# Kernel tuning notes

Measured on AMD Instinct MI355X. Metric: run time of the kernel, lower is better.

## Reference

```python
import jax, jax.numpy as jnp
import numpy as np

N_NODE = 40000  # item vocabulary
H = 100         # hidden size (SR-GNN default)
B = 64          # sessions per batch
L = 16          # items per session (equal-length sessions)
N = B * L       # total graph nodes
E = 2048        # total edges
NL = 1          # GatedGraphConv layers


def setup_inputs() -> dict:
    key = jax.random.key(0)
    ks = jax.random.split(key, 20)
    stdv = 1.0 / np.sqrt(H)
    u = lambda k, shape: jax.random.uniform(k, shape, jnp.float32, -stdv, stdv)
    return {
        "x": jax.random.randint(ks[0], (N,), 0, N_NODE),
        "edge_index": jax.random.randint(ks[1], (2, E), 0, N),
        "edge_weight": jax.random.uniform(ks[2], (E,), jnp.float32),
        "batch": jnp.arange(N) // L,  # node -> session id, equal-length sessions
        "embed": u(ks[3], (N_NODE, H)),
        "ggc_w": u(ks[4], (NL, H, H)),
        "gru_wih": u(ks[5], (3 * H, H)),
        "gru_whh": u(ks[6], (3 * H, H)),
        "gru_bih": u(ks[7], (3 * H,)),
        "gru_bhh": u(ks[8], (3 * H,)),
        "W1_w": u(ks[9], (H, H)), "W1_b": u(ks[10], (H,)),
        "W2_w": u(ks[11], (H, H)), "W2_b": u(ks[12], (H,)),
        "Wt_w": u(ks[13], (H, H)), "Wt_b": u(ks[14], (H,)),
        "q_w": u(ks[15], (1, H)), "q_b": u(ks[16], (1,)),
        "W3_w": u(ks[17], (H, 2 * H)), "W3_b": u(ks[18], (H,)),
    }


def reference(x, edge_index, edge_weight, batch, embed, ggc_w, gru_wih, gru_whh,
              gru_bih, gru_bhh, W1_w, W1_b, W2_w, W2_b, Wt_w, Wt_b, q_w, q_b,
              W3_w, W3_b):
    # Embedding lookup
    h = embed[x]  # [N, H]
    src, dst = edge_index[0], edge_index[1]
    # GatedGraphConv: weighted message aggregation + GRUCell update
    for l in range(NL):
        m = h @ ggc_w[l]                                             # [N, H]
        agg = jnp.zeros_like(h).at[dst].add(edge_weight[:, None] * m[src])
        gi = agg @ gru_wih.T + gru_bih                               # [N, 3H]
        gh = h @ gru_whh.T + gru_bhh
        ir, iz, inn = jnp.split(gi, 3, axis=-1)
        hr, hz, hn = jnp.split(gh, 3, axis=-1)
        r = jax.nn.sigmoid(ir + hr)
        zg = jax.nn.sigmoid(iz + hz)
        ng = jnp.tanh(inn + r * hn)
        h = (1.0 - zg) * ng + zg * h
    v = h.reshape(B, L, H)                                           # sessions
    s_l = v[:, -1]                                                   # [B, H] last item
    # alpha = q(sigmoid(W1(v_n) + W2(v)))
    a = jax.nn.sigmoid((s_l @ W1_w.T + W1_b)[:, None, :] + (v @ W2_w.T + W2_b))
    alpha = a @ q_w.T + q_b                                          # [B, L, 1]
    s_g = jnp.sum(alpha * v, axis=1)                                 # [B, H]
    s_h = jnp.concatenate([s_l, s_g], axis=-1) @ W3_w.T + W3_b       # [B, H]
    # Target attention: s_t[b] = softmax(E @ W_t(v_b)^T, -1) @ v_b, contracted
    # directly against E to avoid materializing [B, N_NODE, H].
    vt = v @ Wt_w.T + Wt_b                                           # [B, L, H]
    P = jax.nn.softmax(jnp.einsum('jh,blh->bjl', embed, vt), axis=-1)
    C = jnp.einsum('blh,jh->bjl', v, embed)                          # v_l . E_j
    z = s_h @ embed.T + jnp.sum(P * C, axis=-1)                      # [B, N_NODE]
    return z
```

## Files before the change

### kernel.cpp

```cpp
#include <hip/hip_runtime.h>
#include <hip/hip_bf16.h>

#define Hh    100
#define NN    1024
#define BB    64
#define LL    16
#define EE    2048
#define NNODE 40000

#define BSPL  8
#define BPB   (BB / BSPL)
#define PFR   12
#define PPAN  (PFR * 64 * 8)

typedef unsigned short u16;
typedef __attribute__((ext_vector_type(8))) short short8;
typedef __attribute__((ext_vector_type(4))) float f32x4;

__device__ __forceinline__ float bf2f(u16 u) {
    union { unsigned int i; float f; } v;
    v.i = ((unsigned int)u) << 16;
    return v.f;
}

__device__ __forceinline__ u16 f2bf(float f) {
    unsigned int x = __float_as_uint(f);
    unsigned int lsb = (x >> 16) & 1u;
    x += 0x7fffu + lsb;
    return (u16)(x >> 16);
}

__device__ __forceinline__ float sigmoidf_(float x) {
    return 1.0f / (1.0f + expf(-x));
}

template <bool BF>
__device__ __forceinline__ float ldv(const void* p, size_t i) {
    if (BF) return bf2f(((const u16*)p)[i]);
    return ((const float*)p)[i];
}
__device__ __forceinline__ float ldvf(int flag, const void* p, size_t i) {
    return flag ? ldv<true>(p, i) : ldv<false>(p, i);
}

template <bool BF>
__device__ void cvt_impl(int t,
                         const void* ew, const void* ggc, const void* wih, const void* whh,
                         const void* bih, const void* bhh, const void* W1w, const void* W1b,
                         const void* W2w, const void* W2b, const void* Wtw, const void* Wtb,
                         const void* qw, const void* qb, const void* W3w, const void* W3b,
                         float* __restrict__ W) {
    const void* src; int si; int doff; int di;
    if      (t <   2048) { src = ew;  si = t;          doff = 0;      di = si; }
    else if (t <  12048) { src = ggc; si = t - 2048;   doff = 2048;   di = si; }
    else if (t <  42048) { src = wih; si = t - 12048;  doff = 12048;  di = (si % 100) * 300 + si / 100; }
    else if (t <  72048) { src = whh; si = t - 42048;  doff = 42048;  di = (si % 100) * 300 + si / 100; }
    else if (t <  72348) { src = bih; si = t - 72048;  doff = 72048;  di = si; }
    else if (t <  72648) { src = bhh; si = t - 72348;  doff = 72352;  di = si; }
    else if (t <  82648) { src = W1w; si = t - 72648;  doff = 72656;  di = (si % 100) * 100 + si / 100; }
    else if (t <  82748) { src = W1b; si = t - 82648;  doff = 82656;  di = si; }
    else if (t <  92748) { src = W2w; si = t - 82748;  doff = 82768;  di = (si % 100) * 100 + si / 100; }
    else if (t <  92848) { src = W2b; si = t - 92748;  doff = 92768;  di = si; }
    else if (t < 102848) { src = Wtw; si = t - 92848;  doff = 92880;  di = (si % 100) * 100 + si / 100; }
    else if (t < 102948) { src = Wtb; si = t - 102848; doff = 102880; di = si; }
    else if (t < 103048) { src = qw;  si = t - 102948; doff = 102992; di = si; }
    else if (t < 103049) { src = qb;  si = t - 103048; doff = 103104; di = si; }
    else if (t < 123049) { src = W3w; si = t - 103049; doff = 103120; di = (si % 200) * 100 + si / 200; }
    else                 { src = W3b; si = t - 123049; doff = 123120; di = si; }
    W[doff + di] = ldv<BF>(src, si);
}

__global__ void __launch_bounds__(256) k_cvt(const void* embed_raw, int* __restrict__ flag,
                      const void* ew, const void* ggc, const void* wih, const void* whh,
                      const void* bih, const void* bhh, const void* W1w, const void* W1b,
                      const void* W2w, const void* W2b, const void* Wtw, const void* Wtb,
                      const void* qw, const void* qb, const void* W3w, const void* W3b,
                      float* __restrict__ W) {
    __shared__ int cnt;
    if (threadIdx.x == 0) cnt = 0;
    __syncthreads();
    int bad = 0;
    const u16* eb = (const u16*)embed_raw;
    for (int i = threadIdx.x; i < 4096; i += 256) {
        float v = bf2f(eb[i]);
        if (!(fabsf(v) <= 0.5f)) bad++;
    }
    if (bad) atomicAdd(&cnt, bad);
    __syncthreads();
    const bool bf = (cnt == 0);
    if (blockIdx.x == 0 && threadIdx.x == 0) flag[0] = bf ? 1 : 0;
    int t = blockIdx.x * 256 + threadIdx.x;
    if (t >= 123149) return;
    if (bf) cvt_impl<true >(t, ew, ggc, wih, whh, bih, bhh, W1w, W1b, W2w, W2b, Wtw, Wtb, qw, qb, W3w, W3b, W);
    else    cvt_impl<false>(t, ew, ggc, wih, whh, bih, bhh, W1w, W1b, W2w, W2b, Wtw, Wtb, qw, qb, W3w, W3b, W);
}

__global__ void __launch_bounds__(256) k_gm(const int* __restrict__ flag,
                                            const int* __restrict__ x,
                                            const void* __restrict__ embed,
                                            const float* __restrict__ ggc_w,
                                            float* __restrict__ m,
                                            float* __restrict__ agg) {
    __shared__ float W[Hh * Hh];
    __shared__ float H[8 * Hh];
    const int tid = threadIdx.x;
    const int fl = flag[0];
    const int r0 = blockIdx.x * 8;
    for (int idx = tid; idx < Hh * Hh; idx += 256) W[idx] = ggc_w[idx];
    for (int idx = tid; idx < 8 * Hh; idx += 256) {
        int i = idx / Hh, j = idx - i * Hh;
        H[idx] = ldvf(fl, embed, (size_t)x[r0 + i] * Hh + j);
    }
    for (int idx = tid; idx < 8 * Hh; idx += 256) agg[r0 * Hh + idx] = 0.0f;
    __syncthreads();
    for (int idx = tid; idx < 8 * Hh; idx += 256) {
        int i = idx / Hh, j = idx - i * Hh;
        float acc = 0.0f;
#pragma unroll 4
        for (int k = 0; k < Hh; ++k) acc += H[i * Hh + k] * W[k * Hh + j];
        m[(r0 + i) * Hh + j] = acc;
    }
}

__global__ void k_scatter(const int* __restrict__ ei, const float* __restrict__ ew,
                          const float* __restrict__ m, float* __restrict__ agg) {
    int t = blockIdx.x * 256 + threadIdx.x;
    if (t >= EE * Hh) return;
    int e = t / Hh, j = t - e * Hh;
    int src = ei[e], dst = ei[EE + e];
    atomicAdd(&agg[dst * Hh + j], ew[e] * m[src * Hh + j]);
}

__global__ void k_gru(const int* __restrict__ flag, const int* __restrict__ x,
                      const void* __restrict__ embed,
                      const float* __restrict__ agg,
                      const float* __restrict__ wihT, const float* __restrict__ whhT,
                      const float* __restrict__ bih, const float* __restrict__ bhh,
                      float* __restrict__ h1) {
    int t = blockIdx.x * 256 + threadIdx.x;
    if (t >= NN * Hh) return;
    int i = t / Hh, j = t - i * Hh;
    const int fl = flag[0];
    const size_t erow = (size_t)x[i] * Hh;
    const float* ar = agg + i * Hh;
    float s_ir = bih[j], s_iz = bih[j + Hh], s_in = bih[j + 2 * Hh];
    float s_hr = bhh[j], s_hz = bhh[j + Hh], s_hn = bhh[j + 2 * Hh];
    float h0j = 0.0f;
    for (int k = 0; k < Hh; ++k) {
        float a = ar[k];
        float h = ldvf(fl, embed, erow + k);
        if (k == j) h0j = h;
        const float* wT = wihT + k * 300;
        const float* uT = whhT + k * 300;
        s_ir += a * wT[j];
        s_iz += a * wT[j + 100];
        s_in += a * wT[j + 200];
        s_hr += h * uT[j];
        s_hz += h * uT[j + 100];
        s_hn += h * uT[j + 200];
    }
    float r = sigmoidf_(s_ir + s_hr);
    float z = sigmoidf_(s_iz + s_hz);
    float n = tanhf(s_in + r * s_hn);
    h1[t] = (1.0f - z) * n + z * h0j;
}

__global__ void __launch_bounds__(256) k_att(const float* __restrict__ h1,
                    const float* __restrict__ W1T, const float* __restrict__ W1b,
                    const float* __restrict__ W2T, const float* __restrict__ W2b,
                    const float* __restrict__ WtT, const float* __restrict__ Wtb,
                    const float* __restrict__ qw, const float* __restrict__ qb,
                    const float* __restrict__ W3T, const float* __restrict__ W3b,
                    u16* __restrict__ P) {
    __shared__ float V[LL * Hh];
    __shared__ float Q2[LL * Hh];
    __shared__ float VTs[LL * Hh];
    __shared__ float Q1[Hh];
    __shared__ float AL[LL];
    __shared__ float SG[Hh];
    __shared__ float SH[Hh];
    const int b = blockIdx.x, tid = threadIdx.x;
    for (int idx = tid; idx < LL * Hh; idx += 256) V[idx] = h1[b * LL * Hh + idx];
    __syncthreads();
    for (int idx = tid; idx < LL * Hh; idx += 256) {
        int i = idx / Hh, j = idx - i * Hh;
        float a2 = 0, at = 0;
        for (int k = 0; k < Hh; ++k) {
            float vk = V[i * Hh + k];
            a2 += vk * W2T[k * Hh + j];
            at += vk * WtT[k * Hh + j];
        }
        Q2[idx] = a2 + W2b[j];
        VTs[idx] = at + Wtb[j];
    }
    if (tid < Hh) {
        float a1 = 0;
        for (int k = 0; k < Hh; ++k) a1 += V[(LL - 1) * Hh + k] * W1T[k * Hh + tid];
        Q1[tid] = a1 + W1b[tid];
    }
    __syncthreads();
    if (tid < LL) {
        float acc = 0;
        for (int j = 0; j < Hh; ++j)
            acc += sigmoidf_(Q1[j] + Q2[tid * Hh + j]) * qw[j];
        AL[tid] = acc + qb[0];
    }
    __syncthreads();
    if (tid < Hh) {
        float acc = 0;
#pragma unroll
        for (int l = 0; l < LL; ++l) acc += AL[l] * V[l * Hh + tid];
        SG[tid] = acc;
    }
    __syncthreads();
    if (tid < Hh) {
        float acc = W3b[tid];
        for (int k = 0; k < Hh; ++k) acc += V[(LL - 1) * Hh + k] * W3T[k * Hh + tid];
        for (int k = 0; k < Hh; ++k) acc += SG[k] * W3T[(Hh + k) * Hh + tid];
        SH[tid] = acc;
    }
    __syncthreads();
    for (int w = tid; w < PFR * 64; w += 256) {
        int f = w >> 6, lane = w & 63;
        int t = f >> 2, ks = f & 3;
        int mm = lane & 15, qq = lane >> 4;
        int row = t * 16 + mm;
        int col0 = ks * 32 + qq * 8;
        short8 t8;
#pragma unroll
        for (int e = 0; e < 8; ++e) {
            int col = col0 + e;
            float v = 0.0f;
            if (col < Hh) {
                if      (row < 16) v = VTs[row * Hh + col];
                else if (row < 32) v = V[(row - 16) * Hh + col];
                else if (row == 32) v = SH[col];
            }
            t8[e] = (short)f2bf(v);
        }
        *(short8*)&P[((size_t)b * PFR + f) * 512 + lane * 8] = t8;
    }
}

__device__ __forceinline__ short8 load_efrag(const void* embed, bool bf, int j, int k0) {
    short8 v = {0, 0, 0, 0, 0, 0, 0, 0};
    if (j >= NNODE || k0 >= Hh) return v;
    if (bf) {
        const u16* row = (const u16*)embed + (size_t)j * Hh + k0;
        if (k0 + 8 <= Hh) {
            ushort4 a = *(const ushort4*)(row);
            ushort4 b = *(const ushort4*)(row + 4);
            v[0] = (short)a.x; v[1] = (short)a.y; v[2] = (short)a.z; v[3] = (short)a.w;
            v[4] = (short)b.x; v[5] = (short)b.y; v[6] = (short)b.z; v[7] = (short)b.w;
        } else {
            for (int e = 0; e < Hh - k0; ++e) v[e] = (short)row[e];
        }
    } else {
        const float* row = (const float*)embed + (size_t)j * Hh + k0;
        if (k0 + 8 <= Hh) {
            float4 a = *(const float4*)(row);
            float4 b = *(const float4*)(row + 4);
            v[0] = (short)f2bf(a.x); v[1] = (short)f2bf(a.y); v[2] = (short)f2bf(a.z); v[3] = (short)f2bf(a.w);
            v[4] = (short)f2bf(b.x); v[5] = (short)f2bf(b.y); v[6] = (short)f2bf(b.z); v[7] = (short)f2bf(b.w);
        } else {
            for (int e = 0; e < Hh - k0; ++e) v[e] = (short)f2bf(row[e]);
        }
    }
    return v;
}

__global__ void __launch_bounds__(256) k_score(const int* __restrict__ flag,
                                               const void* __restrict__ embed,
                                               const u16* __restrict__ P,
                                               void* __restrict__ out) {
    __shared__ alignas(16) u16 sPan[2][PPAN];
    const int jb = blockIdx.x * 128;
    const int b0 = blockIdx.y * BPB;
    const int tid = threadIdx.x;
    const bool bf = (flag[0] != 0);
    const int wave = tid >> 6, lane = tid & 63;
    const int m = lane & 15, quad = lane >> 4;

    short8 Bf[2][4];
#pragma unroll
    for (int g = 0; g < 2; ++g)
#pragma unroll
        for (int ks = 0; ks < 4; ++ks)
            Bf[g][ks] = load_efrag(embed, bf, jb + wave * 32 + g * 16 + m, ks * 32 + quad * 8);

    short8 pa = {0, 0, 0, 0, 0, 0, 0, 0};
    short8 pb = {0, 0, 0, 0, 0, 0, 0, 0};
    if (quad == 0) {
        pa[0] = (short)f2bf((float)m);
        pb[0] = (short)f2bf(1.0f);
    }
    f32x4 pd = (f32x4){0.0f, 0.0f, 0.0f, 0.0f};
    pd = __builtin_amdgcn_mfma_f32_16x16x32_bf16(pa, pb, pd, 0, 0, 0);
    const bool isH1 =
        (__builtin_amdgcn_readfirstlane(__float_as_uint(pd[1])) == 0x3f800000u);

    {
        const uint4* s4 = (const uint4*)(P + (size_t)b0 * PPAN);
        uint4 g0 = s4[tid], g1 = s4[tid + 256], g2 = s4[tid + 512];
        uint4* d = (uint4*)sPan[0];
        d[tid] = g0; d[tid + 256] = g1; d[tid + 512] = g2;
    }
    __syncthreads();

    int cur = 0;
    for (int bi = 0; bi < BPB; ++bi) {
        const int b = b0 + bi;
        uint4 g0, g1, g2;
        if (bi + 1 < BPB) {
            const uint4* s4 = (const uint4*)(P + (size_t)(b + 1) * PPAN);
            g0 = s4[tid]; g1 = s4[tid + 256]; g2 = s4[tid + 512];
        }

        const u16* sp = sPan[cur];
        f32x4 acc[2][3];
#pragma unroll
        for (int g = 0; g < 2; ++g)
#pragma unroll
            for (int t = 0; t < 3; ++t)
                acc[g][t] = (f32x4){0.0f, 0.0f, 0.0f, 0.0f};
#pragma unroll
        for (int t = 0; t < 3; ++t) {
            short8 A0 = *(const short8*)&sp[(t * 4 + 0) * 512 + lane * 8];
            short8 A1 = *(const short8*)&sp[(t * 4 + 1) * 512 + lane * 8];
            short8 A2 = *(const short8*)&sp[(t * 4 + 2) * 512 + lane * 8];
            short8 A3 = *(const short8*)&sp[(t * 4 + 3) * 512 + lane * 8];
#pragma unroll
            for (int g = 0; g < 2; ++g) {
                acc[g][t] = __builtin_amdgcn_mfma_f32_16x16x32_bf16(A0, Bf[g][0], acc[g][t], 0, 0, 0);
                acc[g][t] = __builtin_amdgcn_mfma_f32_16x16x32_bf16(A1, Bf[g][1], acc[g][t], 0, 0, 0);
                acc[g][t] = __builtin_amdgcn_mfma_f32_16x16x32_bf16(A2, Bf[g][2], acc[g][t], 0, 0, 0);
                acc[g][t] = __builtin_amdgcn_mfma_f32_16x16x32_bf16(A3, Bf[g][3], acc[g][t], 0, 0, 0);
            }
        }

#pragma unroll
        for (int g = 0; g < 2; ++g) {
            if (isH1) {
                float den = 0.0f, num = 0.0f;
#pragma unroll
                for (int r = 0; r < 4; ++r) {
                    float p = __expf(acc[g][0][r]);
                    den += p;
                    num += p * acc[g][1][r];
                }
                den += __shfl_xor(den, 16); num += __shfl_xor(num, 16);
                den += __shfl_xor(den, 32); num += __shfl_xor(num, 32);
                if (quad == 0) {
                    int j = jb + wave * 32 + g * 16 + m;
                    if (j < NNODE) {
                        float z = acc[g][2][0] + num / den;
                        if (bf) ((u16*)out)[(size_t)b * NNODE + j] = f2bf(z);
                        else    ((float*)out)[(size_t)b * NNODE + j] = z;
                    }
                }
            } else {
                float den[4], num[4];
#pragma unroll
                for (int r = 0; r < 4; ++r) {
                    float p = __expf(acc[g][0][r]);
                    den[r] = p;
                    num[r] = p * acc[g][1][r];
                }
#pragma unroll
                for (int s = 1; s <= 8; s <<= 1)
#pragma unroll
                    for (int r = 0; r < 4; ++r) {
                        den[r] += __shfl_xor(den[r], s);
                        num[r] += __shfl_xor(num[r], s);
                    }
                if (m == 0) {
#pragma unroll
                    for (int r = 0; r < 4; ++r) {
                        int j = jb + wave * 32 + g * 16 + quad * 4 + r;
                        if (j < NNODE) {
                            float z = acc[g][2][r] + num[r] / den[r];
                            if (bf) ((u16*)out)[(size_t)b * NNODE + j] = f2bf(z);
                            else    ((float*)out)[(size_t)b * NNODE + j] = z;
                        }
                    }
                }
            }
        }

        if (bi + 1 < BPB) {
            uint4* d = (uint4*)sPan[cur ^ 1];
            d[tid] = g0; d[tid + 256] = g1; d[tid + 512] = g2;
        }
        __syncthreads();
        cur ^= 1;
    }
}

extern "C" void kernel_launch(void* const* d_in, const int* in_sizes, int n_in,
                              void* d_out, int out_size, void* d_ws, size_t ws_size,
                              hipStream_t stream) {
    const int* x      = (const int*)d_in[0];
    const int* ei     = (const int*)d_in[1];
    const void* ew    = d_in[2];
    const void* embed = d_in[4];
    const void* ggc   = d_in[5];
    const void* wih   = d_in[6];
    const void* whh   = d_in[7];
    const void* bih   = d_in[8];
    const void* bhh   = d_in[9];
    const void* W1w   = d_in[10];
    const void* W1b   = d_in[11];
    const void* W2w   = d_in[12];
    const void* W2b   = d_in[13];
    const void* Wtw   = d_in[14];
    const void* Wtb   = d_in[15];
    const void* qw    = d_in[16];
    const void* qb    = d_in[17];
    const void* W3w   = d_in[18];
    const void* W3b   = d_in[19];
    float* ws = (float*)d_ws;
    int* flag = (int*)d_ws;

    float* W = ws + 64;
    float* ew_f  = W + 0;
    float* ggc_f = W + 2048;
    float* wihT  = W + 12048;
    float* whhT  = W + 42048;
    float* bih_f = W + 72048;
    float* bhh_f = W + 72352;
    float* W1T   = W + 72656;
    float* W1b_f = W + 82656;
    float* W2T   = W + 82768;
    float* W2b_f = W + 92768;
    float* WtT   = W + 92880;
    float* Wtb_f = W + 102880;
    float* qw_f  = W + 102992;
    float* qb_f  = W + 103104;
    float* W3T   = W + 103120;
    float* W3b_f = W + 123120;

    float* D     = ws + 123296;
    float* m     = D;
    float* agg   = D + 102400;
    float* h1    = D;
    u16*   P     = (u16*)(D + 102400);

    k_cvt    <<<dim3(482), dim3(256), 0, stream>>>(embed, flag, ew, ggc, wih, whh, bih, bhh,
                                                   W1w, W1b, W2w, W2b, Wtw, Wtb, qw, qb, W3w, W3b, W);
    k_gm     <<<dim3(128), dim3(256), 0, stream>>>(flag, x, embed, ggc_f, m, agg);
    k_scatter<<<dim3(800), dim3(256), 0, stream>>>(ei, ew_f, m, agg);
    k_gru    <<<dim3(400), dim3(256), 0, stream>>>(flag, x, embed, agg, wihT, whhT, bih_f, bhh_f, h1);
    k_att    <<<dim3(64),  dim3(256), 0, stream>>>(h1, W1T, W1b_f, W2T, W2b_f, WtT, Wtb_f,
                                                   qw_f, qb_f, W3T, W3b_f, P);
    k_score  <<<dim3((NNODE + 127) / 128, BSPL), dim3(256), 0, stream>>>(flag, embed, P, d_out);
}
```

Baseline: 234.6 us.

## Fuse all six stages into one cooperative persistent kernel with grid syncs

Replaces the six separate kernel launches with a single cooperative kernel that runs each stage as a grid-stride loop separated by grid.sync(). The scoring stage becomes a persistent job loop over (node tile, batch split) pairs. The goal is to remove the launch gaps between the short stages. In exchange, every block repeats the bf16 detection check, the gm stage no longer caches weights in shared memory, and grid-wide barriers add their own cost.

```diff
diff --git a/kernel.cpp b/kernel.cpp
--- a/kernel.cpp
+++ b/kernel.cpp
@@ -1,5 +1,8 @@
 #include <hip/hip_runtime.h>
+#include <hip/hip_cooperative_groups.h>
 #include <hip/hip_bf16.h>
+
+namespace cg = cooperative_groups;
 
 #define Hh    100
 #define NN    1024
@@ -12,6 +15,8 @@
 #define BPB   (BB / BSPL)
 #define PFR   12
 #define PPAN  (PFR * 64 * 8)
+#define NJT   313
+#define NJOB  (NJT * BSPL)
 
 typedef unsigned short u16;
 typedef __attribute__((ext_vector_type(8))) short short8;
@@ -39,8 +44,8 @@
     if (BF) return bf2f(((const u16*)p)[i]);
     return ((const float*)p)[i];
 }
-__device__ __forceinline__ float ldvf(int flag, const void* p, size_t i) {
-    return flag ? ldv<true>(p, i) : ldv<false>(p, i);
+__device__ __forceinline__ float ldvb(bool bf, const void* p, size_t i) {
+    return bf ? ldv<true>(p, i) : ldv<false>(p, i);
 }
 
 template <bool BF>
@@ -70,178 +75,6 @@
     W[doff + di] = ldv<BF>(src, si);
 }
 
-__global__ void __launch_bounds__(256) k_cvt(const void* embed_raw, int* __restrict__ flag,
-                      const void* ew, const void* ggc, const void* wih, const void* whh,
-                      const void* bih, const void* bhh, const void* W1w, const void* W1b,
-                      const void* W2w, const void* W2b, const void* Wtw, const void* Wtb,
-                      const void* qw, const void* qb, const void* W3w, const void* W3b,
-                      float* __restrict__ W) {
-    __shared__ int cnt;
-    if (threadIdx.x == 0) cnt = 0;
-    __syncthreads();
-    int bad = 0;
-    const u16* eb = (const u16*)embed_raw;
-    for (int i = threadIdx.x; i < 4096; i += 256) {
-        float v = bf2f(eb[i]);
-        if (!(fabsf(v) <= 0.5f)) bad++;
-    }
-    if (bad) atomicAdd(&cnt, bad);
-    __syncthreads();
-    const bool bf = (cnt == 0);
-    if (blockIdx.x == 0 && threadIdx.x == 0) flag[0] = bf ? 1 : 0;
-    int t = blockIdx.x * 256 + threadIdx.x;
-    if (t >= 123149) return;
-    if (bf) cvt_impl<true >(t, ew, ggc, wih, whh, bih, bhh, W1w, W1b, W2w, W2b, Wtw, Wtb, qw, qb, W3w, W3b, W);
-    else    cvt_impl<false>(t, ew, ggc, wih, whh, bih, bhh, W1w, W1b, W2w, W2b, Wtw, Wtb, qw, qb, W3w, W3b, W);
-}
-
-__global__ void __launch_bounds__(256) k_gm(const int* __restrict__ flag,
-                                            const int* __restrict__ x,
-                                            const void* __restrict__ embed,
-                                            const float* __restrict__ ggc_w,
-                                            float* __restrict__ m,
-                                            float* __restrict__ agg) {
-    __shared__ float W[Hh * Hh];
-    __shared__ float H[8 * Hh];
-    const int tid = threadIdx.x;
-    const int fl = flag[0];
-    const int r0 = blockIdx.x * 8;
-    for (int idx = tid; idx < Hh * Hh; idx += 256) W[idx] = ggc_w[idx];
-    for (int idx = tid; idx < 8 * Hh; idx += 256) {
-        int i = idx / Hh, j = idx - i * Hh;
-        H[idx] = ldvf(fl, embed, (size_t)x[r0 + i] * Hh + j);
-    }
-    for (int idx = tid; idx < 8 * Hh; idx += 256) agg[r0 * Hh + idx] = 0.0f;
-    __syncthreads();
-    for (int idx = tid; idx < 8 * Hh; idx += 256) {
-        int i = idx / Hh, j = idx - i * Hh;
-        float acc = 0.0f;
-#pragma unroll 4
-        for (int k = 0; k < Hh; ++k) acc += H[i * Hh + k] * W[k * Hh + j];
-        m[(r0 + i) * Hh + j] = acc;
-    }
-}
-
-__global__ void k_scatter(const int* __restrict__ ei, const float* __restrict__ ew,
-                          const float* __restrict__ m, float* __restrict__ agg) {
-    int t = blockIdx.x * 256 + threadIdx.x;
-    if (t >= EE * Hh) return;
-    int e = t / Hh, j = t - e * Hh;
-    int src = ei[e], dst = ei[EE + e];
-    atomicAdd(&agg[dst * Hh + j], ew[e] * m[src * Hh + j]);
-}
-
-__global__ void k_gru(const int* __restrict__ flag, const int* __restrict__ x,
-                      const void* __restrict__ embed,
-                      const float* __restrict__ agg,
-                      const float* __restrict__ wihT, const float* __restrict__ whhT,
-                      const float* __restrict__ bih, const float* __restrict__ bhh,
-                      float* __restrict__ h1) {
-    int t = blockIdx.x * 256 + threadIdx.x;
-    if (t >= NN * Hh) return;
-    int i = t / Hh, j = t - i * Hh;
-    const int fl = flag[0];
-    const size_t erow = (size_t)x[i] * Hh;
-    const float* ar = agg + i * Hh;
-    float s_ir = bih[j], s_iz = bih[j + Hh], s_in = bih[j + 2 * Hh];
-    float s_hr = bhh[j], s_hz = bhh[j + Hh], s_hn = bhh[j + 2 * Hh];
-    float h0j = 0.0f;
-    for (int k = 0; k < Hh; ++k) {
-        float a = ar[k];
-        float h = ldvf(fl, embed, erow + k);
-        if (k == j) h0j = h;
-        const float* wT = wihT + k * 300;
-        const float* uT = whhT + k * 300;
-        s_ir += a * wT[j];
-        s_iz += a * wT[j + 100];
-        s_in += a * wT[j + 200];
-        s_hr += h * uT[j];
-        s_hz += h * uT[j + 100];
-        s_hn += h * uT[j + 200];
-    }
-    float r = sigmoidf_(s_ir + s_hr);
-    float z = sigmoidf_(s_iz + s_hz);
-    float n = tanhf(s_in + r * s_hn);
-    h1[t] = (1.0f - z) * n + z * h0j;
-}
-
-__global__ void __launch_bounds__(256) k_att(const float* __restrict__ h1,
-                    const float* __restrict__ W1T, const float* __restrict__ W1b,
-                    const float* __restrict__ W2T, const float* __restrict__ W2b,
-                    const float* __restrict__ WtT, const float* __restrict__ Wtb,
-                    const float* __restrict__ qw, const float* __restrict__ qb,
-                    const float* __restrict__ W3T, const float* __restrict__ W3b,
-                    u16* __restrict__ P) {
-    __shared__ float V[LL * Hh];
-    __shared__ float Q2[LL * Hh];
-    __shared__ float VTs[LL * Hh];
-    __shared__ float Q1[Hh];
-    __shared__ float AL[LL];
-    __shared__ float SG[Hh];
-    __shared__ float SH[Hh];
-    const int b = blockIdx.x, tid = threadIdx.x;
-    for (int idx = tid; idx < LL * Hh; idx += 256) V[idx] = h1[b * LL * Hh + idx];
-    __syncthreads();
-    for (int idx = tid; idx < LL * Hh; idx += 256) {
-        int i = idx / Hh, j = idx - i * Hh;
-        float a2 = 0, at = 0;
-        for (int k = 0; k < Hh; ++k) {
-            float vk = V[i * Hh + k];
-            a2 += vk * W2T[k * Hh + j];
-            at += vk * WtT[k * Hh + j];
-        }
-        Q2[idx] = a2 + W2b[j];
-        VTs[idx] = at + Wtb[j];
-    }
-    if (tid < Hh) {
-        float a1 = 0;
-        for (int k = 0; k < Hh; ++k) a1 += V[(LL - 1) * Hh + k] * W1T[k * Hh + tid];
-        Q1[tid] = a1 + W1b[tid];
-    }
-    __syncthreads();
-    if (tid < LL) {
-        float acc = 0;
-        for (int j = 0; j < Hh; ++j)
-            acc += sigmoidf_(Q1[j] + Q2[tid * Hh + j]) * qw[j];
-        AL[tid] = acc + qb[0];
-    }
-    __syncthreads();
-    if (tid < Hh) {
-        float acc = 0;
-#pragma unroll
-        for (int l = 0; l < LL; ++l) acc += AL[l] * V[l * Hh + tid];
-        SG[tid] = acc;
-    }
-    __syncthreads();
-    if (tid < Hh) {
-        float acc = W3b[tid];
-        for (int k = 0; k < Hh; ++k) acc += V[(LL - 1) * Hh + k] * W3T[k * Hh + tid];
-        for (int k = 0; k < Hh; ++k) acc += SG[k] * W3T[(Hh + k) * Hh + tid];
-        SH[tid] = acc;
-    }
-    __syncthreads();
-    for (int w = tid; w < PFR * 64; w += 256) {
-        int f = w >> 6, lane = w & 63;
-        int t = f >> 2, ks = f & 3;
-        int mm = lane & 15, qq = lane >> 4;
-        int row = t * 16 + mm;
-        int col0 = ks * 32 + qq * 8;
-        short8 t8;
-#pragma unroll
-        for (int e = 0; e < 8; ++e) {
-            int col = col0 + e;
-            float v = 0.0f;
-            if (col < Hh) {
-                if      (row < 16) v = VTs[row * Hh + col];
-                else if (row < 32) v = V[(row - 16) * Hh + col];
-                else if (row == 32) v = SH[col];
-            }
-            t8[e] = (short)f2bf(v);
-        }
-        *(short8*)&P[((size_t)b * PFR + f) * 512 + lane * 8] = t8;
-    }
-}
-
 __device__ __forceinline__ short8 load_efrag(const void* embed, bool bf, int j, int k0) {
     short8 v = {0, 0, 0, 0, 0, 0, 0, 0};
     if (j >= NNODE || k0 >= Hh) return v;
@@ -269,29 +102,192 @@
     return v;
 }
 
-__global__ void __launch_bounds__(256) k_score(const int* __restrict__ flag,
-                                               const void* __restrict__ embed,
-                                               const u16* __restrict__ P,
-                                               void* __restrict__ out) {
-    __shared__ alignas(16) u16 sPan[2][PPAN];
-    const int jb = blockIdx.x * 128;
-    const int b0 = blockIdx.y * BPB;
-    const int tid = threadIdx.x;
-    const bool bf = (flag[0] != 0);
+__global__ void __launch_bounds__(256) mega(
+        const int* __restrict__ x, const int* __restrict__ ei,
+        const void* __restrict__ ew, const void* __restrict__ embed,
+        const void* __restrict__ ggc, const void* __restrict__ wih,
+        const void* __restrict__ whh, const void* __restrict__ bih,
+        const void* __restrict__ bhh, const void* __restrict__ W1w,
+        const void* __restrict__ W1b, const void* __restrict__ W2w,
+        const void* __restrict__ W2b, const void* __restrict__ Wtw,
+        const void* __restrict__ Wtb, const void* __restrict__ qw,
+        const void* __restrict__ qb, const void* __restrict__ W3w,
+        const void* __restrict__ W3b, float* __restrict__ ws,
+        void* __restrict__ out) {
+    cg::grid_group grid = cg::this_grid();
+    __shared__ alignas(16) unsigned char smraw[2 * PPAN * 2];
+    __shared__ int cnt;
+    const int tid = threadIdx.x, bid = blockIdx.x, nb = gridDim.x;
+    const int gtid = bid * 256 + tid, gsz = nb * 256;
+
+    if (tid == 0) cnt = 0;
+    __syncthreads();
+    {
+        const u16* eb = (const u16*)embed;
+        int bad = 0;
+        for (int i = tid; i < 4096; i += 256) {
+            float v = bf2f(eb[i]);
+            if (!(fabsf(v) <= 0.5f)) bad++;
+        }
+        if (bad) atomicAdd(&cnt, bad);
+    }
+    __syncthreads();
+    const bool bf = (cnt == 0);
+
+    float* W = ws + 64;
+    const float* ew_f  = W + 0;
+    const float* ggc_f = W + 2048;
+    const float* wihT  = W + 12048;
+    const float* whhT  = W + 42048;
+    const float* bih_f = W + 72048;
+    const float* bhh_f = W + 72352;
+    const float* W1T   = W + 72656;
+    const float* W1b_f = W + 82656;
+    const float* W2T   = W + 82768;
+    const float* W2b_f = W + 92768;
+    const float* WtT   = W + 92880;
+    const float* Wtb_f = W + 102880;
+    const float* qw_f  = W + 102992;
+    const float* qb_f  = W + 103104;
+    const float* W3T   = W + 103120;
+    const float* W3b_f = W + 123120;
+    float* D   = ws + 123296;
+    float* m   = D;
+    float* agg = D + 102400;
+    float* h1  = D;
+    u16*   P   = (u16*)(D + 102400);
+
+    for (int t = gtid; t < 123149; t += gsz) {
+        if (bf) cvt_impl<true >(t, ew, ggc, wih, whh, bih, bhh, W1w, W1b, W2w, W2b, Wtw, Wtb, qw, qb, W3w, W3b, W);
+        else    cvt_impl<false>(t, ew, ggc, wih, whh, bih, bhh, W1w, W1b, W2w, W2b, Wtw, Wtb, qw, qb, W3w, W3b, W);
+    }
+    grid.sync();
+
+    for (int t = gtid; t < NN * Hh; t += gsz) {
+        int i = t / Hh, j = t - i * Hh;
+        size_t er = (size_t)x[i] * Hh;
+        float acc = 0.0f;
+#pragma unroll 4
+        for (int k = 0; k < Hh; ++k) acc += ldvb(bf, embed, er + k) * ggc_f[k * Hh + j];
+        m[t] = acc;
+        agg[t] = 0.0f;
+    }
+    grid.sync();
+
+    for (int t = gtid; t < EE * Hh; t += gsz) {
+        int e = t / Hh, j = t - e * Hh;
+        atomicAdd(&agg[ei[EE + e] * Hh + j], ew_f[e] * m[ei[e] * Hh + j]);
+    }
+    grid.sync();
+
+    for (int t = gtid; t < NN * Hh; t += gsz) {
+        int i = t / Hh, j = t - i * Hh;
+        const size_t erow = (size_t)x[i] * Hh;
+        const float* ar = agg + i * Hh;
+        float s_ir = bih_f[j], s_iz = bih_f[j + Hh], s_in = bih_f[j + 2 * Hh];
+        float s_hr = bhh_f[j], s_hz = bhh_f[j + Hh], s_hn = bhh_f[j + 2 * Hh];
+        float h0j = 0.0f;
+        for (int k = 0; k < Hh; ++k) {
+            float a = ar[k];
+            float h = ldvb(bf, embed, erow + k);
+            if (k == j) h0j = h;
+            const float* wT = wihT + k * 300;
+            const float* uT = whhT + k * 300;
+            s_ir += a * wT[j];
+            s_iz += a * wT[j + 100];
+            s_in += a * wT[j + 200];
+            s_hr += h * uT[j];
+            s_hz += h * uT[j + 100];
+            s_hn += h * uT[j + 200];
+        }
+        float r = sigmoidf_(s_ir + s_hr);
+        float z = sigmoidf_(s_iz + s_hz);
+        float n = tanhf(s_in + r * s_hn);
+        h1[t] = (1.0f - z) * n + z * h0j;
+    }
+    grid.sync();
+
+    if (bid < BB) {
+        float* V   = (float*)smraw;
+        float* Q2  = V + 1600;
+        float* VTs = Q2 + 1600;
+        float* Q1  = VTs + 1600;
+        float* AL  = Q1 + 100;
+        float* SG  = AL + 16;
+        float* SH  = SG + 100;
+        const int b = bid;
+        for (int idx = tid; idx < LL * Hh; idx += 256) V[idx] = h1[b * LL * Hh + idx];
+        __syncthreads();
+        for (int idx = tid; idx < LL * Hh; idx += 256) {
+            int i = idx / Hh, j = idx - i * Hh;
+            float a2 = 0, at = 0;
+            for (int k = 0; k < Hh; ++k) {
+                float vk = V[i * Hh + k];
+                a2 += vk * W2T[k * Hh + j];
+                at += vk * WtT[k * Hh + j];
+            }
+            Q2[idx] = a2 + W2b_f[j];
+            VTs[idx] = at + Wtb_f[j];
+        }
+        if (tid < Hh) {
+            float a1 = 0;
+            for (int k = 0; k < Hh; ++k) a1 += V[(LL - 1) * Hh + k] * W1T[k * Hh + tid];
+            Q1[tid] = a1 + W1b_f[tid];
+        }
+        __syncthreads();
+        if (tid < LL) {
+            float acc = 0;
+            for (int j = 0; j < Hh; ++j)
+                acc += sigmoidf_(Q1[j] + Q2[tid * Hh + j]) * qw_f[j];
+            AL[tid] = acc + qb_f[0];
+        }
+        __syncthreads();
+        if (tid < Hh) {
+            float acc = 0;
+#pragma unroll
+            for (int l = 0; l < LL; ++l) acc += AL[l] * V[l * Hh + tid];
+            SG[tid] = acc;
+        }
+        __syncthreads();
+        if (tid < Hh) {
+            float acc = W3b_f[tid];
+            for (int k = 0; k < Hh; ++k) acc += V[(LL - 1) * Hh + k] * W3T[k * Hh + tid];
+            for (int k = 0; k < Hh; ++k) acc += SG[k] * W3T[(Hh + k) * Hh + tid];
+            SH[tid] = acc;
+        }
+        __syncthreads();
+        for (int w = tid; w < PFR * 64; w += 256) {
+            int f = w >> 6, lane = w & 63;
+            int t = f >> 2, ks = f & 3;
+            int mm = lane & 15, qq = lane >> 4;
+            int row = t * 16 + mm;
+            int col0 = ks * 32 + qq * 8;
+            short8 t8;
+#pragma unroll
+            for (int e = 0; e < 8; ++e) {
+                int col = col0 + e;
+                float v = 0.0f;
+                if (col < Hh) {
+                    if      (row < 16) v = VTs[row * Hh + col];
+                    else if (row < 32) v = V[(row - 16) * Hh + col];
+                    else if (row == 32) v = SH[col];
+                }
+                t8[e] = (short)f2bf(v);
+            }
+            *(short8*)&P[((size_t)b * PFR + f) * 512 + lane * 8] = t8;
+        }
+        __syncthreads();
+    }
+    grid.sync();
+
+    u16 (*sPan)[PPAN] = (u16 (*)[PPAN])smraw;
     const int wave = tid >> 6, lane = tid & 63;
-    const int m = lane & 15, quad = lane >> 4;
-
-    short8 Bf[2][4];
-#pragma unroll
-    for (int g = 0; g < 2; ++g)
-#pragma unroll
-        for (int ks = 0; ks < 4; ++ks)
-            Bf[g][ks] = load_efrag(embed, bf, jb + wave * 32 + g * 16 + m, ks * 32 + quad * 8);
+    const int mq = lane & 15, quad = lane >> 4;
 
     short8 pa = {0, 0, 0, 0, 0, 0, 0, 0};
     short8 pb = {0, 0, 0, 0, 0, 0, 0, 0};
     if (quad == 0) {
-        pa[0] = (short)f2bf((float)m);
+        pa[0] = (short)f2bf((float)mq);
         pb[0] = (short)f2bf(1.0f);
     }
     f32x4 pd = (f32x4){0.0f, 0.0f, 0.0f, 0.0f};
@@ -299,100 +295,112 @@
     const bool isH1 =
         (__builtin_amdgcn_readfirstlane(__float_as_uint(pd[1])) == 0x3f800000u);
 
-    {
-        const uint4* s4 = (const uint4*)(P + (size_t)b0 * PPAN);
-        uint4 g0 = s4[tid], g1 = s4[tid + 256], g2 = s4[tid + 512];
-        uint4* d = (uint4*)sPan[0];
-        d[tid] = g0; d[tid + 256] = g1; d[tid + 512] = g2;
-    }
-    __syncthreads();
-
-    int cur = 0;
-    for (int bi = 0; bi < BPB; ++bi) {
-        const int b = b0 + bi;
-        uint4 g0, g1, g2;
-        if (bi + 1 < BPB) {
-            const uint4* s4 = (const uint4*)(P + (size_t)(b + 1) * PPAN);
-            g0 = s4[tid]; g1 = s4[tid + 256]; g2 = s4[tid + 512];
-        }
-
-        const u16* sp = sPan[cur];
-        f32x4 acc[2][3];
+    for (int job = bid; job < NJOB; job += nb) {
+        const int jb = (job % NJT) * 128;
+        const int b0 = (job / NJT) * BPB;
+
+        short8 Bf[2][4];
 #pragma unroll
         for (int g = 0; g < 2; ++g)
 #pragma unroll
-            for (int t = 0; t < 3; ++t)
-                acc[g][t] = (f32x4){0.0f, 0.0f, 0.0f, 0.0f};
-#pragma unroll
-        for (int t = 0; t < 3; ++t) {
-            short8 A0 = *(const short8*)&sp[(t * 4 + 0) * 512 + lane * 8];
-            short8 A1 = *(const short8*)&sp[(t * 4 + 1) * 512 + lane * 8];
-            short8 A2 = *(const short8*)&sp[(t * 4 + 2) * 512 + lane * 8];
-            short8 A3 = *(const short8*)&sp[(t * 4 + 3) * 512 + lane * 8];
+            for (int ks = 0; ks < 4; ++ks)
+                Bf[g][ks] = load_efrag(embed, bf, jb + wave * 32 + g * 16 + mq, ks * 32 + quad * 8);
+
+        {
+            const uint4* s4 = (const uint4*)(P + (size_t)b0 * PPAN);
+            uint4 g0 = s4[tid], g1 = s4[tid + 256], g2 = s4[tid + 512];
+            uint4* d = (uint4*)sPan[0];
+            d[tid] = g0; d[tid + 256] = g1; d[tid + 512] = g2;
+        }
+        __syncthreads();
+
+        int cur = 0;
+        for (int bi = 0; bi < BPB; ++bi) {
+            const int b = b0 + bi;
+            uint4 g0, g1, g2;
+            if (bi + 1 < BPB) {
+                const uint4* s4 = (const uint4*)(P + (size_t)(b + 1) * PPAN);
+                g0 = s4[tid]; g1 = s4[tid + 256]; g2 = s4[tid + 512];
+            }
+
+            const u16* sp = sPan[cur];
+            f32x4 acc[2][3];
+#pragma unroll
+            for (int g = 0; g < 2; ++g)
+#pragma unroll
+                for (int t = 0; t < 3; ++t)
+                    acc[g][t] = (f32x4){0.0f, 0.0f, 0.0f, 0.0f};
+#pragma unroll
+            for (int t = 0; t < 3; ++t) {
+                short8 A0 = *(const short8*)&sp[(t * 4 + 0) * 512 + lane * 8];
+                short8 A1 = *(const short8*)&sp[(t * 4 + 1) * 512 + lane * 8];
+                short8 A2 = *(const short8*)&sp[(t * 4 + 2) * 512 + lane * 8];
+                short8 A3 = *(const short8*)&sp[(t * 4 + 3) * 512 + lane * 8];
+#pragma unroll
+                for (int g = 0; g < 2; ++g) {
+                    acc[g][t] = __builtin_amdgcn_mfma_f32_16x16x32_bf16(A0, Bf[g][0], acc[g][t], 0, 0, 0);
+                    acc[g][t] = __builtin_amdgcn_mfma_f32_16x16x32_bf16(A1, Bf[g][1], acc[g][t], 0, 0, 0);
+                    acc[g][t] = __builtin_amdgcn_mfma_f32_16x16x32_bf16(A2, Bf[g][2], acc[g][t], 0, 0, 0);
+                    acc[g][t] = __builtin_amdgcn_mfma_f32_16x16x32_bf16(A3, Bf[g][3], acc[g][t], 0, 0, 0);
+                }
+            }
+
 #pragma unroll
             for (int g = 0; g < 2; ++g) {
-                acc[g][t] = __builtin_amdgcn_mfma_f32_16x16x32_bf16(A0, Bf[g][0], acc[g][t], 0, 0, 0);
-                acc[g][t] = __builtin_amdgcn_mfma_f32_16x16x32_bf16(A1, Bf[g][1], acc[g][t], 0, 0, 0);
-                acc[g][t] = __builtin_amdgcn_mfma_f32_16x16x32_bf16(A2, Bf[g][2], acc[g][t], 0, 0, 0);
-                acc[g][t] = __builtin_amdgcn_mfma_f32_16x16x32_bf16(A3, Bf[g][3], acc[g][t], 0, 0, 0);
-            }
-        }
-
-#pragma unroll
-        for (int g = 0; g < 2; ++g) {
-            if (isH1) {
-                float den = 0.0f, num = 0.0f;
-#pragma unroll
-                for (int r = 0; r < 4; ++r) {
-                    float p = __expf(acc[g][0][r]);
-                    den += p;
-                    num += p * acc[g][1][r];
-                }
-                den += __shfl_xor(den, 16); num += __shfl_xor(num, 16);
-                den += __shfl_xor(den, 32); num += __shfl_xor(num, 32);
-                if (quad == 0) {
-                    int j = jb + wave * 32 + g * 16 + m;
-                    if (j < NNODE) {
-                        float z = acc[g][2][0] + num / den;
-                        if (bf) ((u16*)out)[(size_t)b * NNODE + j] = f2bf(z);
-                        else    ((float*)out)[(size_t)b * NNODE + j] = z;
+                if (isH1) {
+                    float den = 0.0f, num = 0.0f;
+#pragma unroll
+                    for (int r = 0; r < 4; ++r) {
+                        float p = __expf(acc[g][0][r]);
+                        den += p;
+                        num += p * acc[g][1][r];
                     }
-                }
-            } else {
-                float den[4], num[4];
-#pragma unroll
-                for (int r = 0; r < 4; ++r) {
-                    float p = __expf(acc[g][0][r]);
-                    den[r] = p;
-                    num[r] = p * acc[g][1][r];
-                }
-#pragma unroll
-                for (int s = 1; s <= 8; s <<= 1)
-#pragma unroll
-                    for (int r = 0; r < 4; ++r) {
-                        den[r] += __shfl_xor(den[r], s);
-                        num[r] += __shfl_xor(num[r], s);
-                    }
-                if (m == 0) {
-#pragma unroll
-                    for (int r = 0; r < 4; ++r) {
-                        int j = jb + wave * 32 + g * 16 + quad * 4 + r;
+                    den += __shfl_xor(den, 16); num += __shfl_xor(num, 16);
+                    den += __shfl_xor(den, 32); num += __shfl_xor(num, 32);
+                    if (quad == 0) {
+                        int j = jb + wave * 32 + g * 16 + mq;
                         if (j < NNODE) {
-                            float z = acc[g][2][r] + num[r] / den[r];
+                            float z = acc[g][2][0] + num / den;
                             if (bf) ((u16*)out)[(size_t)b * NNODE + j] = f2bf(z);
                             else    ((float*)out)[(size_t)b * NNODE + j] = z;
                         }
                     }
+                } else {
+                    float den[4], num[4];
+#pragma unroll
+                    for (int r = 0; r < 4; ++r) {
+                        float p = __expf(acc[g][0][r]);
+                        den[r] = p;
+                        num[r] = p * acc[g][1][r];
+                    }
+#pragma unroll
+                    for (int s = 1; s <= 8; s <<= 1)
+#pragma unroll
+                        for (int r = 0; r < 4; ++r) {
+                            den[r] += __shfl_xor(den[r], s);
+                            num[r] += __shfl_xor(num[r], s);
+                        }
+                    if (mq == 0) {
+#pragma unroll
+                        for (int r = 0; r < 4; ++r) {
+                            int j = jb + wave * 32 + g * 16 + quad * 4 + r;
+                            if (j < NNODE) {
+                                float z = acc[g][2][r] + num[r] / den[r];
+                                if (bf) ((u16*)out)[(size_t)b * NNODE + j] = f2bf(z);
+                                else    ((float*)out)[(size_t)b * NNODE + j] = z;
+                            }
+                        }
+                    }
                 }
             }
-        }
-
-        if (bi + 1 < BPB) {
-            uint4* d = (uint4*)sPan[cur ^ 1];
-            d[tid] = g0; d[tid + 256] = g1; d[tid + 512] = g2;
-        }
-        __syncthreads();
-        cur ^= 1;
+
+            if (bi + 1 < BPB) {
+                uint4* d = (uint4*)sPan[cur ^ 1];
+                d[tid] = g0; d[tid + 256] = g1; d[tid + 512] = g2;
+            }
+            __syncthreads();
+            cur ^= 1;
+        }
     }
 }
 
@@ -419,38 +427,23 @@
     const void* W3w   = d_in[18];
     const void* W3b   = d_in[19];
     float* ws = (float*)d_ws;
-    int* flag = (int*)d_ws;
-
-    float* W = ws + 64;
-    float* ew_f  = W + 0;
-    float* ggc_f = W + 2048;
-    float* wihT  = W + 12048;
-    float* whhT  = W + 42048;
-    float* bih_f = W + 72048;
-    float* bhh_f = W + 72352;
-    float* W1T   = W + 72656;
-    float* W1b_f = W + 82656;
-    float* W2T   = W + 82768;
-    float* W2b_f = W + 92768;
-    float* WtT   = W + 92880;
-    float* Wtb_f = W + 102880;
-    float* qw_f  = W + 102992;
-    float* qb_f  = W + 103104;
-    float* W3T   = W + 103120;
-    float* W3b_f = W + 123120;
-
-    float* D     = ws + 123296;
-    float* m     = D;
-    float* agg   = D + 102400;
-    float* h1    = D;
-    u16*   P     = (u16*)(D + 102400);
-
-    k_cvt    <<<dim3(482), dim3(256), 0, stream>>>(embed, flag, ew, ggc, wih, whh, bih, bhh,
-                                                   W1w, W1b, W2w, W2b, Wtw, Wtb, qw, qb, W3w, W3b, W);
-    k_gm     <<<dim3(128), dim3(256), 0, stream>>>(flag, x, embed, ggc_f, m, agg);
-    k_scatter<<<dim3(800), dim3(256), 0, stream>>>(ei, ew_f, m, agg);
-    k_gru    <<<dim3(400), dim3(256), 0, stream>>>(flag, x, embed, agg, wihT, whhT, bih_f, bhh_f, h1);
-    k_att    <<<dim3(64),  dim3(256), 0, stream>>>(h1, W1T, W1b_f, W2T, W2b_f, WtT, Wtb_f,
-                                                   qw_f, qb_f, W3T, W3b_f, P);
-    k_score  <<<dim3((NNODE + 127) / 128, BSPL), dim3(256), 0, stream>>>(flag, embed, P, d_out);
-}
+    void* out = d_out;
+
+    int perCU = 0;
+    if (hipOccupancyMaxActiveBlocksPerMultiprocessor(&perCU, (const void*)mega, 256, 0)
+            != hipSuccess || perCU <= 0)
+        perCU = 2;
+    long long g = (long long)perCU * 256;
+    if (g > NJOB) g = NJOB;
+    if (g < BB)   g = BB;
+    dim3 gridDim((unsigned)g), blockDim(256);
+
+    void* args[] = {
+        (void*)&x, (void*)&ei, (void*)&ew, (void*)&embed, (void*)&ggc,
+        (void*)&wih, (void*)&whh, (void*)&bih, (void*)&bhh,
+        (void*)&W1w, (void*)&W1b, (void*)&W2w, (void*)&W2b,
+        (void*)&Wtw, (void*)&Wtb, (void*)&qw, (void*)&qb,
+        (void*)&W3w, (void*)&W3b, (void*)&ws, (void*)&out
+    };
+    hipLaunchCooperativeKernel((const void*)mega, gridDim, blockDim, args, 0, stream);
+}
```

After: 493.8 us. 2.1x slower.
